# Optimization experiments

Measured on AMD Instinct MI355X. Metric: run time of the kernel, lower is better.

## Reference

```python
import jax, jax.numpy as jnp
import numpy as np

NB_CLASSES = 100
SZ_EMBED = 512
BATCH = 512
MRG = 0.1


def setup_inputs() -> dict:
    key = jax.random.key(0)
    k1, k2 = jax.random.split(key)
    X = jax.random.normal(k1, (BATCH, SZ_EMBED), dtype=jnp.float32)
    labels = jax.random.randint(k2, (BATCH,), 0, NB_CLASSES, dtype=jnp.int64)
    mu = jnp.ones((NB_CLASSES,), dtype=jnp.float32) * MRG
    nv = jnp.ones((NB_CLASSES,), dtype=jnp.float32) * MRG
    return {"X": X, "labels": labels, "mu": mu, "nv": nv}


def reference(X, labels, mu, nv):
    # D[i,j] = <x_i, x_j>  (F.linear(X, X) == X @ X.T)
    D = jnp.einsum("id,jd->ij", X, X)  # [B, B]
    B = X.shape[0]
    n_classes = mu.shape[0]

    same = labels[:, None] == labels[None, :]          # [B, B]
    eye = jnp.eye(B, dtype=bool)
    pos = same & (~eye)                                 # valid positives j for anchor i
    neg = ~same                                         # valid negatives k for anchor i

    mu_i = mu[labels]                                   # per-anchor margin [B]
    # T[i,j,k] = D[i,j] - D[i,k] + mu[labels[i]]
    T = D[:, :, None] - D[:, None, :] + mu_i[:, None, None]  # [B, B, B]
    valid = pos[:, :, None] & neg[:, None, :]                # [B, B, B]
    hinge_sum = jnp.sum(jnp.where(valid, jnp.maximum(T, 0.0), 0.0))

    # margin regularizers: -sum(mu)/C - sum(nv)/C
    return hinge_sum - jnp.sum(mu) / n_classes - jnp.sum(nv) / n_classes
```

## Files before the change

### kernel.cpp

```cpp
#include <hip/hip_runtime.h>

#define BATCH 512
#define EMBED 512
#define BLOCK 256
#define TS 32
#define KSPLIT 2


__global__ __launch_bounds__(256) void gram_gemm(
    const float* __restrict__ X, float* __restrict__ Dp, float* __restrict__ out)
{
    if (blockIdx.x == 0 && blockIdx.y == 0 && blockIdx.z == 0 && threadIdx.x == 0)
        *out = 0.0f;

    __shared__ float As[TS][TS + 4];
    __shared__ float Bs[TS][TS + 4];

    const int tid   = threadIdx.x;
    const int row0  = blockIdx.y * TS;
    const int col0  = blockIdx.x * TS;
    const int kbase = blockIdx.z * (EMBED / KSPLIT);

    const int lr = tid >> 3;
    const int lc = (tid & 7) << 2;
    const int ty = tid >> 4;
    const int tx = tid & 15;

    float acc00 = 0.f, acc01 = 0.f, acc10 = 0.f, acc11 = 0.f;

    for (int kc = kbase; kc < kbase + EMBED / KSPLIT; kc += TS) {
        *(float4*)&As[lr][lc] = *(const float4*)(X + (size_t)(row0 + lr) * EMBED + kc + lc);
        *(float4*)&Bs[lr][lc] = *(const float4*)(X + (size_t)(col0 + lr) * EMBED + kc + lc);
        __syncthreads();

#pragma unroll
        for (int kk = 0; kk < TS; kk += 4) {
            float4 a0 = *(float4*)&As[ty][kk];
            float4 a1 = *(float4*)&As[ty + 16][kk];
            float4 b0 = *(float4*)&Bs[tx][kk];
            float4 b1 = *(float4*)&Bs[tx + 16][kk];
            acc00 = fmaf(a0.x, b0.x, acc00); acc00 = fmaf(a0.y, b0.y, acc00);
            acc00 = fmaf(a0.z, b0.z, acc00); acc00 = fmaf(a0.w, b0.w, acc00);
            acc01 = fmaf(a0.x, b1.x, acc01); acc01 = fmaf(a0.y, b1.y, acc01);
            acc01 = fmaf(a0.z, b1.z, acc01); acc01 = fmaf(a0.w, b1.w, acc01);
            acc10 = fmaf(a1.x, b0.x, acc10); acc10 = fmaf(a1.y, b0.y, acc10);
            acc10 = fmaf(a1.z, b0.z, acc10); acc10 = fmaf(a1.w, b0.w, acc10);
            acc11 = fmaf(a1.x, b1.x, acc11); acc11 = fmaf(a1.y, b1.y, acc11);
            acc11 = fmaf(a1.z, b1.z, acc11); acc11 = fmaf(a1.w, b1.w, acc11);
        }
        __syncthreads();
    }

    float* O = Dp + (size_t)blockIdx.z * BATCH * BATCH
                  + (size_t)(row0 + ty) * BATCH + col0 + tx;
    O[0]  = acc00;
    O[16] = acc01;
    O += (size_t)16 * BATCH;
    O[0]  = acc10;
    O[16] = acc11;
}

__global__ __launch_bounds__(BLOCK) void hinge_reduce(
    const float* __restrict__ Dp,
    const int* __restrict__ labels,
    const float* __restrict__ mu,
    const float* __restrict__ nv,
    float* __restrict__ out,
    int n_classes)
{
    __shared__ float drow[BATCH];
    __shared__ int   lab[BATCH];
    __shared__ int   poslist[BATCH];
    __shared__ float dijmu[BATCH];
    __shared__ int   npos_s;
    __shared__ float red[BLOCK / 64];

    const int i = blockIdx.x;
    const int tid = threadIdx.x;
    const int wave = tid >> 6;
    const int lane = tid & 63;

    if (tid == 0) npos_s = 0;
    for (int t = tid; t < BATCH; t += BLOCK) lab[t] = labels[t];
    if (tid < BATCH / 4) {
        float4 d0 = ((const float4*)(Dp + (size_t)i * BATCH))[tid];
        float4 d1 = ((const float4*)(Dp + (size_t)BATCH * BATCH + (size_t)i * BATCH))[tid];
        float4 s; s.x = d0.x + d1.x; s.y = d0.y + d1.y; s.z = d0.z + d1.z; s.w = d0.w + d1.w;
        ((float4*)drow)[tid] = s;
    }
    __syncthreads();

    const int li = lab[i];
    const float mu_i = mu[li];

    for (int t = tid; t < BATCH; t += BLOCK) {
        if (t != i && lab[t] == li) {
            int idx = atomicAdd(&npos_s, 1);
            poslist[idx] = t;
        }
    }
    __syncthreads();
    const int npos = npos_s;
    for (int t = tid; t < npos; t += BLOCK)
        dijmu[t] = drow[poslist[t]] + mu_i;
    __syncthreads();

    float local = 0.0f;
#pragma unroll
    for (int kk = 0; kk < BATCH / BLOCK; ++kk) {
        int k = tid + kk * BLOCK;
        if (lab[k] != li) {
            float dk = drow[k];
            for (int p = 0; p < npos; ++p)
                local += fmaxf(dijmu[p] - dk, 0.0f);
        }
    }

    if (i == 0 && tid < n_classes)
        local -= (mu[tid] + nv[tid]) / (float)n_classes;

    for (int off = 32; off > 0; off >>= 1)
        local += __shfl_down(local, off, 64);
    if (lane == 0) red[wave] = local;
    __syncthreads();
    if (tid == 0) {
        float s = 0.f;
        for (int w = 0; w < BLOCK / 64; ++w) s += red[w];
        atomicAdd(out, s);
    }
}

extern "C" void kernel_launch(void* const* d_in, const int* in_sizes, int n_in,
                              void* d_out, int out_size, void* d_ws, size_t ws_size,
                              hipStream_t stream) {
    const float* X      = (const float*)d_in[0];
    const int*   labels = (const int*)d_in[1];
    const float* mu     = (const float*)d_in[2];
    const float* nv     = (const float*)d_in[3];
    float* out = (float*)d_out;
    float* Dp  = (float*)d_ws;
    const int n_classes = in_sizes[2];

    dim3 ggrid(BATCH / TS, BATCH / TS, KSPLIT);
    gram_gemm<<<ggrid, dim3(256), 0, stream>>>(X, Dp, out);

    hinge_reduce<<<dim3(BATCH), dim3(BLOCK), 0, stream>>>(
        Dp, labels, mu, nv, out, n_classes);
}
```

Baseline: 79.50 us.

## Fuse Gram computation into hinge kernel, two anchors per block

Replaces the split-K tiled GEMM plus separate hinge reduction with a single kernel. Each block computes the two Gram rows it needs directly from X, holding the two anchor rows in registers and reducing dot products with wave shuffles. The hinge sum for both anchors then runs from shared memory. This removes the workspace round trip and the second launch, but every block now streams all of X from global/L2, so the total GEMM work is redone per anchor pair. The output is zeroed with a memset instead of inside the kernel.

```diff
diff --git a/kernel.cpp b/kernel.cpp
--- a/kernel.cpp
+++ b/kernel.cpp
@@ -1,149 +1,133 @@
 #include <hip/hip_runtime.h>
 
-#define BATCH 512
-#define EMBED 512
-#define BLOCK 256
-#define TS 32
-#define KSPLIT 2
+#define BATCH   512
+#define EMBED   512
+#define NF4     (EMBED / 4)
+#define THREADS 512
+#define GANCH   2
 
+__global__ __launch_bounds__(THREADS) void fused_loss(
+    const float* __restrict__ X,
+    const int*   __restrict__ labels,
+    const float* __restrict__ mu,
+    const float* __restrict__ nv,
+    float*       __restrict__ out,
+    int n_classes)
+{
+    __shared__ float d0[BATCH];
+    __shared__ float d1[BATCH];
+    __shared__ float dijmu0[BATCH];
+    __shared__ float dijmu1[BATCH];
+    __shared__ int   lab[BATCH];
+    __shared__ int   npos0_s, npos1_s;
+    __shared__ float red[THREADS / 64];
 
-__global__ __launch_bounds__(256) void gram_gemm(
-    const float* __restrict__ X, float* __restrict__ Dp, float* __restrict__ out)
-{
-    if (blockIdx.x == 0 && blockIdx.y == 0 && blockIdx.z == 0 && threadIdx.x == 0)
-        *out = 0.0f;
+    const int tid  = threadIdx.x;
+    const int lane = tid & 63;
+    const int wave = tid >> 6;
+    const int sub  = lane & 7;
+    const int rg   = lane >> 3;
+    const int i0   = blockIdx.x * GANCH;
+    const int i1   = i0 + 1;
 
-    __shared__ float As[TS][TS + 4];
-    __shared__ float Bs[TS][TS + 4];
+    lab[tid] = labels[tid];
+    if (tid == 0) { npos0_s = 0; npos1_s = 0; }
 
-    const int tid   = threadIdx.x;
-    const int row0  = blockIdx.y * TS;
-    const int col0  = blockIdx.x * TS;
-    const int kbase = blockIdx.z * (EMBED / KSPLIT);
+    const float4* __restrict__ X4 = (const float4*)X;
+    const float4* __restrict__ A0 = X4 + (size_t)i0 * NF4;
+    const float4* __restrict__ A1 = X4 + (size_t)i1 * NF4;
 
-    const int lr = tid >> 3;
-    const int lc = (tid & 7) << 2;
-    const int ty = tid >> 4;
-    const int tx = tid & 15;
-
-    float acc00 = 0.f, acc01 = 0.f, acc10 = 0.f, acc11 = 0.f;
-
-    for (int kc = kbase; kc < kbase + EMBED / KSPLIT; kc += TS) {
-        *(float4*)&As[lr][lc] = *(const float4*)(X + (size_t)(row0 + lr) * EMBED + kc + lc);
-        *(float4*)&Bs[lr][lc] = *(const float4*)(X + (size_t)(col0 + lr) * EMBED + kc + lc);
-        __syncthreads();
-
+    float4 a0[16], a1[16];
 #pragma unroll
-        for (int kk = 0; kk < TS; kk += 4) {
-            float4 a0 = *(float4*)&As[ty][kk];
-            float4 a1 = *(float4*)&As[ty + 16][kk];
-            float4 b0 = *(float4*)&Bs[tx][kk];
-            float4 b1 = *(float4*)&Bs[tx + 16][kk];
-            acc00 = fmaf(a0.x, b0.x, acc00); acc00 = fmaf(a0.y, b0.y, acc00);
-            acc00 = fmaf(a0.z, b0.z, acc00); acc00 = fmaf(a0.w, b0.w, acc00);
-            acc01 = fmaf(a0.x, b1.x, acc01); acc01 = fmaf(a0.y, b1.y, acc01);
-            acc01 = fmaf(a0.z, b1.z, acc01); acc01 = fmaf(a0.w, b1.w, acc01);
-            acc10 = fmaf(a1.x, b0.x, acc10); acc10 = fmaf(a1.y, b0.y, acc10);
-            acc10 = fmaf(a1.z, b0.z, acc10); acc10 = fmaf(a1.w, b0.w, acc10);
-            acc11 = fmaf(a1.x, b1.x, acc11); acc11 = fmaf(a1.y, b1.y, acc11);
-            acc11 = fmaf(a1.z, b1.z, acc11); acc11 = fmaf(a1.w, b1.w, acc11);
-        }
-        __syncthreads();
+    for (int c = 0; c < 16; ++c) {
+        a0[c] = A0[c * 8 + sub];
+        a1[c] = A1[c * 8 + sub];
     }
 
-    float* O = Dp + (size_t)blockIdx.z * BATCH * BATCH
-                  + (size_t)(row0 + ty) * BATCH + col0 + tx;
-    O[0]  = acc00;
-    O[16] = acc01;
-    O += (size_t)16 * BATCH;
-    O[0]  = acc10;
-    O[16] = acc11;
-}
+#pragma unroll 1
+    for (int pass = 0; pass < 8; ++pass) {
+        const int r = (wave << 6) + (pass << 3) + rg;
+        const float4* __restrict__ Xr = X4 + (size_t)r * NF4;
+        float acc0 = 0.f, acc1 = 0.f;
+#pragma unroll
+        for (int c = 0; c < 16; ++c) {
+            const float4 x = Xr[c * 8 + sub];
+            acc0 = fmaf(x.x, a0[c].x, acc0);
+            acc0 = fmaf(x.y, a0[c].y, acc0);
+            acc0 = fmaf(x.z, a0[c].z, acc0);
+            acc0 = fmaf(x.w, a0[c].w, acc0);
+            acc1 = fmaf(x.x, a1[c].x, acc1);
+            acc1 = fmaf(x.y, a1[c].y, acc1);
+            acc1 = fmaf(x.z, a1[c].z, acc1);
+            acc1 = fmaf(x.w, a1[c].w, acc1);
+        }
+#pragma unroll
+        for (int off = 1; off <= 4; off <<= 1) {
+            acc0 += __shfl_xor(acc0, off, 64);
+            acc1 += __shfl_xor(acc1, off, 64);
+        }
+        if (sub == 0) { d0[r] = acc0; d1[r] = acc1; }
+    }
 
-__global__ __launch_bounds__(BLOCK) void hinge_reduce(
-    const float* __restrict__ Dp,
-    const int* __restrict__ labels,
-    const float* __restrict__ mu,
-    const float* __restrict__ nv,
-    float* __restrict__ out,
-    int n_classes)
-{
-    __shared__ float drow[BATCH];
-    __shared__ int   lab[BATCH];
-    __shared__ int   poslist[BATCH];
-    __shared__ float dijmu[BATCH];
-    __shared__ int   npos_s;
-    __shared__ float red[BLOCK / 64];
+    __syncthreads();
 
-    const int i = blockIdx.x;
-    const int tid = threadIdx.x;
-    const int wave = tid >> 6;
-    const int lane = tid & 63;
+    const int   l0  = lab[i0];
+    const int   l1  = lab[i1];
+    const float mu0 = mu[l0];
+    const float mu1 = mu[l1];
 
-    if (tid == 0) npos_s = 0;
-    for (int t = tid; t < BATCH; t += BLOCK) lab[t] = labels[t];
-    if (tid < BATCH / 4) {
-        float4 d0 = ((const float4*)(Dp + (size_t)i * BATCH))[tid];
-        float4 d1 = ((const float4*)(Dp + (size_t)BATCH * BATCH + (size_t)i * BATCH))[tid];
-        float4 s; s.x = d0.x + d1.x; s.y = d0.y + d1.y; s.z = d0.z + d1.z; s.w = d0.w + d1.w;
-        ((float4*)drow)[tid] = s;
+    if (tid != i0 && lab[tid] == l0) {
+        int p = atomicAdd(&npos0_s, 1);
+        dijmu0[p] = d0[tid] + mu0;
+    }
+    if (tid != i1 && lab[tid] == l1) {
+        int p = atomicAdd(&npos1_s, 1);
+        dijmu1[p] = d1[tid] + mu1;
     }
     __syncthreads();
 
-    const int li = lab[i];
-    const float mu_i = mu[li];
+    const int npos0 = npos0_s;
+    const int npos1 = npos1_s;
 
-    for (int t = tid; t < BATCH; t += BLOCK) {
-        if (t != i && lab[t] == li) {
-            int idx = atomicAdd(&npos_s, 1);
-            poslist[idx] = t;
-        }
-    }
-    __syncthreads();
-    const int npos = npos_s;
-    for (int t = tid; t < npos; t += BLOCK)
-        dijmu[t] = drow[poslist[t]] + mu_i;
-    __syncthreads();
+    float local = 0.f;
+    const float dk0 = d0[tid];
+    const float dk1 = d1[tid];
+    if (lab[tid] != l0)
+        for (int p = 0; p < npos0; ++p)
+            local += fmaxf(dijmu0[p] - dk0, 0.f);
+    if (lab[tid] != l1)
+        for (int p = 0; p < npos1; ++p)
+            local += fmaxf(dijmu1[p] - dk1, 0.f);
 
-    float local = 0.0f;
-#pragma unroll
-    for (int kk = 0; kk < BATCH / BLOCK; ++kk) {
-        int k = tid + kk * BLOCK;
-        if (lab[k] != li) {
-            float dk = drow[k];
-            for (int p = 0; p < npos; ++p)
-                local += fmaxf(dijmu[p] - dk, 0.0f);
-        }
-    }
-
-    if (i == 0 && tid < n_classes)
+    if (blockIdx.x == 0 && tid < n_classes)
         local -= (mu[tid] + nv[tid]) / (float)n_classes;
 
+#pragma unroll
     for (int off = 32; off > 0; off >>= 1)
         local += __shfl_down(local, off, 64);
     if (lane == 0) red[wave] = local;
     __syncthreads();
     if (tid == 0) {
         float s = 0.f;
-        for (int w = 0; w < BLOCK / 64; ++w) s += red[w];
+#pragma unroll
+        for (int w = 0; w < THREADS / 64; ++w) s += red[w];
         atomicAdd(out, s);
     }
 }
 
 extern "C" void kernel_launch(void* const* d_in, const int* in_sizes, int n_in,
                               void* d_out, int out_size, void* d_ws, size_t ws_size,
-                              hipStream_t stream) {
+                              hipStream_t stream)
+{
     const float* X      = (const float*)d_in[0];
     const int*   labels = (const int*)d_in[1];
     const float* mu     = (const float*)d_in[2];
     const float* nv     = (const float*)d_in[3];
     float* out = (float*)d_out;
-    float* Dp  = (float*)d_ws;
     const int n_classes = in_sizes[2];
 
-    dim3 ggrid(BATCH / TS, BATCH / TS, KSPLIT);
-    gram_gemm<<<ggrid, dim3(256), 0, stream>>>(X, Dp, out);
+    hipMemsetAsync(d_out, 0, sizeof(float), stream);
 
-    hinge_reduce<<<dim3(BATCH), dim3(BLOCK), 0, stream>>>(
-        Dp, labels, mu, nv, out, n_classes);
+    fused_loss<<<dim3(BATCH / GANCH), dim3(THREADS), 0, stream>>>(
+        X, labels, mu, nv, out, n_classes);
 }
```

After: 104.0 us. 30.8% more time.
